# Optimization experiments

Hardware: AMD Instinct MI355X
Metric: run time of the kernel (lower is better)

Reference implementation:

```python
import jax, jax.numpy as jnp
import numpy as np

QMIN, QMAX = -128.0, 127.0

def _affine_quantize(x):
    # per-tensor asymmetric int8 activation quantization
    amin, amax = jnp.min(x), jnp.max(x)
    scale = jnp.maximum((amax - amin) / 255.0, 1e-8)
    zp = jnp.clip(jnp.round(-amin / scale) + QMIN, QMIN, QMAX)
    q = jnp.clip(jnp.round(x / scale) + zp, QMIN, QMAX)
    return q, scale, zp

def _sym_quantize(w):
    # per-tensor symmetric int8 weight quantization
    scale = jnp.maximum(jnp.max(jnp.abs(w)) / 127.0, 1e-8)
    q = jnp.clip(jnp.round(w / scale), -127.0, 127.0)
    return q, scale

def _qlinear(x, W, b):
    # quantize input -> integer GEMM (emulated in fp32) -> dequantize
    xq, sx, zx = _affine_quantize(x)
    wq, sw = _sym_quantize(W)
    acc = jnp.einsum('bsh,oh->bso', xq - zx, wq)  # int accumulate, fp32-emulated
    return acc * (sx * sw) + b


def setup_inputs() -> dict:
    key = jax.random.key(0)
    k1, k2, k3, k4, k5 = jax.random.split(key, 5)
    d, h = 1024, 4096
    x = jax.random.normal(k1, (4, 4096, d), dtype=jnp.float32)
    W1 = jax.random.normal(k2, (h, d), dtype=jnp.float32) * (1.0 / np.sqrt(d))
    b1 = jax.random.normal(k3, (h,), dtype=jnp.float32) * 0.02
    W2 = jax.random.normal(k4, (d, h), dtype=jnp.float32) * (1.0 / np.sqrt(h))
    b2 = jax.random.normal(k5, (d,), dtype=jnp.float32) * 0.02
    return {"x": x, "W1": W1, "b1": b1, "W2": W2, "b2": b2}


def reference(x, W1, b1, W2, b2):
    # 1. FP32 -> quantize -> INT8 fc1 -> dequantize -> FP32
    h = _qlinear(x, W1, b1)
    # 2. FP32 GELU (torch nn.GELU default: exact erf form); dropout p=0 is identity
    h = jax.nn.gelu(h, approximate=False)
    # 3. FP32 -> quantize -> INT8 fc2 -> dequantize -> FP32
    out = _qlinear(h, W2, b2)
    return out
```

## Files before the change

### kernel.cpp

```cpp
#include <hip/hip_runtime.h>
#include <hip/hip_bf16.h>
#include <math.h>

#define D_IN   1024
#define D_HID  4096
#define M_TOK  16384

typedef int v4i __attribute__((ext_vector_type(4)));
typedef _Float16 f16x8 __attribute__((ext_vector_type(8)));

typedef __attribute__((address_space(3))) unsigned int lds_u32;
typedef const __attribute__((address_space(1))) unsigned int glb_u32;

__device__ inline void gload_lds16(const signed char* g, signed char* l) {
    __builtin_amdgcn_global_load_lds((glb_u32*)g, (lds_u32*)l, 16, 0, 0);
}

__device__ inline float fast_erf(float x) {
    float ax = fabsf(x);
    float t = __builtin_amdgcn_rcpf(fmaf(0.3275911f, ax, 1.0f));
    float y = t * (0.254829592f +
              t * (-0.284496736f +
              t * (1.421413741f +
              t * (-1.453152027f +
              t * 1.061405429f))));
    float e = __expf(-ax * ax);
    float r = fmaf(-y, e, 1.0f);
    return copysignf(r, x);
}

#define OFF_SLOTS  ((size_t)0)
#define OFF_SCAL   ((size_t)64)
#define OFF_ISCAL  ((size_t)128)
#define OFF_XQ     ((size_t)256)
#define OFF_W1Q    (OFF_XQ  + (size_t)M_TOK * D_IN)
#define OFF_W2Q    (OFF_W1Q + (size_t)D_HID * D_IN)
#define OFF_RS1    (OFF_W2Q + (size_t)D_IN * D_HID)
#define OFF_RS2    (OFF_RS1 + (size_t)D_HID * 4)
#define OFF_H      (OFF_RS2 + (size_t)D_IN * 4 + 128)
#define OFF_HQ     (OFF_H   + (size_t)M_TOK * D_HID * 2)


__device__ inline unsigned enc_f(float f) {
    unsigned u = __float_as_uint(f);
    return (u & 0x80000000u) ? ~u : (u | 0x80000000u);
}
__device__ inline float dec_f(unsigned u) {
    return __uint_as_float((u & 0x80000000u) ? (u ^ 0x80000000u) : ~u);
}

__global__ void k_reduce_all(const float4* __restrict__ x,
                             const float4* __restrict__ w1,
                             const float4* __restrict__ w2,
                             float* __restrict__ pxmin, float* __restrict__ pxmax,
                             float* __restrict__ pw1, float* __restrict__ pw2) {
    __shared__ float red[8];
    const int b = blockIdx.x;
    const int wave = threadIdx.x >> 6, lane = threadIdx.x & 63;
    if (b < 1024) {
        float vmin = 3.4e38f, vmax = -3.4e38f;
        for (int i = b * 256 + threadIdx.x; i < M_TOK * D_IN / 4; i += 1024 * 256) {
            float4 v = x[i];
            vmin = fminf(vmin, fminf(fminf(v.x, v.y), fminf(v.z, v.w)));
            vmax = fmaxf(vmax, fmaxf(fmaxf(v.x, v.y), fmaxf(v.z, v.w)));
        }
        for (int off = 32; off > 0; off >>= 1) {
            vmin = fminf(vmin, __shfl_down(vmin, off));
            vmax = fmaxf(vmax, __shfl_down(vmax, off));
        }
        if (lane == 0) { red[wave] = vmin; red[4 + wave] = vmax; }
        __syncthreads();
        if (threadIdx.x == 0) {
            pxmin[b] = fminf(fminf(red[0], red[1]), fminf(red[2], red[3]));
            pxmax[b] = fmaxf(fmaxf(red[4], red[5]), fmaxf(red[6], red[7]));
        }
    } else {
        const float4* w = (b < 1280) ? w1 : w2;
        const int bb = (b < 1280) ? b - 1024 : b - 1280;
        float vmax = 0.0f;
        for (int i = bb * 256 + threadIdx.x; i < D_HID * D_IN / 4; i += 256 * 256) {
            float4 v = w[i];
            vmax = fmaxf(vmax, fmaxf(fmaxf(fabsf(v.x), fabsf(v.y)), fmaxf(fabsf(v.z), fabsf(v.w))));
        }
        for (int off = 32; off > 0; off >>= 1)
            vmax = fmaxf(vmax, __shfl_down(vmax, off));
        if (lane == 0) red[wave] = vmax;
        __syncthreads();
        if (threadIdx.x == 0) {
            float bm = fmaxf(fmaxf(red[0], red[1]), fmaxf(red[2], red[3]));
            if (b < 1280) pw1[bb] = bm; else pw2[bb] = bm;
        }
    }
}

__global__ void k_quant_all(const float4* __restrict__ x, int* __restrict__ xq,
                            const float* __restrict__ W1, signed char* __restrict__ w1q,
                            int* __restrict__ rs1,
                            const float* __restrict__ W2, signed char* __restrict__ w2q,
                            int* __restrict__ rs2,
                            const float* __restrict__ pxmin, const float* __restrict__ pxmax,
                            const float* __restrict__ pw1, const float* __restrict__ pw2,
                            float* __restrict__ scal, int* __restrict__ iscal,
                            unsigned* __restrict__ slots) {
    __shared__ float sred[8];
    __shared__ int red[4];
    const int b = blockIdx.x;
    const int wave = threadIdx.x >> 6, lane = threadIdx.x & 63;

    if (b < 2048) {
        float vmin = 3.4e38f, vmax = -3.4e38f;
        for (int i = threadIdx.x; i < 1024; i += 256) {
            vmin = fminf(vmin, pxmin[i]);
            vmax = fmaxf(vmax, pxmax[i]);
        }
        for (int off = 32; off > 0; off >>= 1) {
            vmin = fminf(vmin, __shfl_down(vmin, off));
            vmax = fmaxf(vmax, __shfl_down(vmax, off));
        }
        if (lane == 0) { sred[wave] = vmin; sred[4 + wave] = vmax; }
        __syncthreads();
        vmin = fminf(fminf(sred[0], sred[1]), fminf(sred[2], sred[3]));
        vmax = fmaxf(fmaxf(sred[4], sred[5]), fmaxf(sred[6], sred[7]));
        float s = fmaxf((vmax - vmin) / 255.0f, 1e-8f);
        float zp = rintf(-vmin / s) - 128.0f;
        zp = fminf(fmaxf(zp, -128.0f), 127.0f);

        if (b == 0 && threadIdx.x == 0) {
            float w1m = 0.0f, w2m = 0.0f;
            for (int i = 0; i < 256; i++) {
                w1m = fmaxf(w1m, pw1[i]);
                w2m = fmaxf(w2m, pw2[i]);
            }
            float sw1 = fmaxf(w1m / 127.0f, 1e-8f);
            float sw2 = fmaxf(w2m / 127.0f, 1e-8f);
            scal[0] = s; scal[1] = zp; scal[2] = sw1; scal[3] = sw2; scal[4] = s * sw1;
            iscal[0] = (int)zp;
            slots[4] = 0xFFFFFFFFu;
            slots[5] = 0u;
        }

        for (int i = b * 256 + threadIdx.x; i < M_TOK * D_IN / 4; i += 2048 * 256) {
            float4 v = x[i];
            int a0 = (int)fminf(fmaxf(rintf(v.x / s) + zp, -128.0f), 127.0f);
            int a1 = (int)fminf(fmaxf(rintf(v.y / s) + zp, -128.0f), 127.0f);
            int a2 = (int)fminf(fmaxf(rintf(v.z / s) + zp, -128.0f), 127.0f);
            int a3 = (int)fminf(fmaxf(rintf(v.w / s) + zp, -128.0f), 127.0f);
            xq[i] = (a0 & 255) | ((a1 & 255) << 8) | ((a2 & 255) << 16) | ((a3 & 255) << 24);
        }
        return;
    }

    const int isW1 = (b < 2048 + 4096);
    const int row = isW1 ? (b - 2048) : (b - 6144);
    const int K = isW1 ? D_IN : D_HID;
    const float* pw = isW1 ? pw1 : pw2;
    const float* W = isW1 ? W1 : W2;
    signed char* Wq = isW1 ? w1q : w2q;
    int* rsum = isW1 ? rs1 : rs2;

    float wm = pw[threadIdx.x & 255];
    for (int off = 32; off > 0; off >>= 1)
        wm = fmaxf(wm, __shfl_down(wm, off));
    if (lane == 0) sred[wave] = wm;
    __syncthreads();
    wm = fmaxf(fmaxf(sred[0], sred[1]), fmaxf(sred[2], sred[3]));
    const float s = fmaxf(wm / 127.0f, 1e-8f);

    const float4* Wr = (const float4*)(W + (size_t)row * K);
    int* out = (int*)(Wq + (size_t)row * K);
    int mysum = 0;
    for (int i = threadIdx.x; i < K / 4; i += 256) {
        float4 v = Wr[i];
        int a0 = (int)fminf(fmaxf(rintf(v.x / s), -127.0f), 127.0f);
        int a1 = (int)fminf(fmaxf(rintf(v.y / s), -127.0f), 127.0f);
        int a2 = (int)fminf(fmaxf(rintf(v.z / s), -127.0f), 127.0f);
        int a3 = (int)fminf(fmaxf(rintf(v.w / s), -127.0f), 127.0f);
        mysum += a0 + a1 + a2 + a3;
        out[i] = (a0 & 255) | ((a1 & 255) << 8) | ((a2 & 255) << 16) | ((a3 & 255) << 24);
    }
    for (int off = 32; off > 0; off >>= 1)
        mysum += __shfl_down(mysum, off);
    if (lane == 0) red[wave] = mysum;
    __syncthreads();
    if (threadIdx.x == 0) rsum[row] = red[0] + red[1] + red[2] + red[3];
}

__global__ void k_quant_h(const f16x8* __restrict__ H, int2* __restrict__ Hq, int n8,
                          const unsigned* __restrict__ slots) {
    float amin = dec_f(slots[4]), amax = dec_f(slots[5]);
    float s = fmaxf((amax - amin) / 255.0f, 1e-8f);
    float zp = rintf(-amin / s) - 128.0f;
    zp = fminf(fmaxf(zp, -128.0f), 127.0f);
    for (int i = blockIdx.x * blockDim.x + threadIdx.x; i < n8; i += gridDim.x * blockDim.x) {
        f16x8 v = H[i];
        int q[8];
#pragma unroll
        for (int j = 0; j < 8; j++)
            q[j] = ((int)fminf(fmaxf(rintf((float)v[j] / s) + zp, -128.0f), 127.0f)) & 255;
        int lo = q[0] | (q[1] << 8) | (q[2] << 16) | (q[3] << 24);
        int hi = q[4] | (q[5] << 8) | (q[6] << 16) | (q[7] << 24);
        Hq[i] = make_int2(lo, hi);
    }
}

__device__ inline void int8_mainloop256(const signed char* __restrict__ A,
                                        const signed char* __restrict__ B,
                                        int K, int m0, int n0,
                                        signed char* Ls, v4i (&acc)[8][4]) {
    const int tid = threadIdx.x;
    const int l = tid & 63, w = tid >> 6;
    const int lm = l & 15, lq = l >> 4;
    const int wmi = w >> 1, wni = w & 1;

    const int gc16 = ((l & 3) ^ ((l >> 3) & 3)) << 4;
    const int srow = (w << 4) + (l >> 2);
    const signed char* gA = A + (long)(m0 + srow) * K + gc16;
    const signed char* gB = B + (long)(n0 + srow) * K + gc16;
    const long rstep = (long)K << 6;
    signed char* lA = Ls + (w << 10) + (l << 4);
    signed char* lB = Ls + 16384 + (w << 10) + (l << 4);

    const int f16off = (lq ^ ((lm >> 1) & 3)) << 4;
    const int aoff = ((wmi << 7) + lm) * 64 + f16off;
    const int boff = 16384 + ((wni << 6) + lm) * 64 + f16off;

    const int KT = K >> 6;

    auto stage = [&](int bufoff, int kt) {
        const signed char* a = gA + ((long)kt << 6);
        const signed char* b = gB + ((long)kt << 6);
        gload_lds16(a,             lA + bufoff);
        gload_lds16(a + rstep,     lA + bufoff + 4096);
        gload_lds16(a + 2 * rstep, lA + bufoff + 8192);
        gload_lds16(a + 3 * rstep, lA + bufoff + 12288);
        gload_lds16(b,             lB + bufoff);
        gload_lds16(b + rstep,     lB + bufoff + 4096);
    };

    auto compute = [&](int bufoff) {
        v4i av[8], bv[4];
#pragma unroll
        for (int j = 0; j < 4; ++j)
            bv[j] = *(const v4i*)&Ls[bufoff + boff + j * 1024];
#pragma unroll
        for (int i = 0; i < 8; ++i)
            av[i] = *(const v4i*)&Ls[bufoff + aoff + i * 1024];
        __builtin_amdgcn_s_setprio(1);
#pragma unroll
        for (int i = 0; i < 8; ++i)
#pragma unroll
            for (int j = 0; j < 4; ++j)
                acc[i][j] = __builtin_amdgcn_mfma_i32_16x16x64_i8(av[i], bv[j], acc[i][j], 0, 0, 0);
        __builtin_amdgcn_s_setprio(0);
    };

    stage(0, 0);
    stage(24576, 1);

    int b0 = 0, b1 = 24576, b2 = 49152;
    for (int t = 0; t < KT - 2; ++t) {
        asm volatile("s_waitcnt vmcnt(6)\n\ts_barrier" ::: "memory");
        stage(b2, t + 2);
        compute(b0);
        int tmp = b0; b0 = b1; b1 = b2; b2 = tmp;
    }
    asm volatile("s_waitcnt vmcnt(6)\n\ts_barrier" ::: "memory");
    compute(b0);
    asm volatile("s_waitcnt vmcnt(0)\n\ts_barrier" ::: "memory");
    compute(b1);
}

__global__ __launch_bounds__(256, 2) void k_gemm1(const signed char* __restrict__ Aq,
                                                  const signed char* __restrict__ Bq,
                                                  _Float16* __restrict__ H,
                                                  const float* __restrict__ scal,
                                                  const int* __restrict__ iscal,
                                                  const int* __restrict__ rsum,
                                                  const float* __restrict__ bias,
                                                  unsigned* slots) {
    __shared__ __align__(16) signed char Ls[3 * 24576];
    __shared__ float red[8];
    const int nb = D_HID / 128;
    const int m0 = (blockIdx.x / nb) * 256, n0 = (blockIdx.x % nb) * 128;
    v4i acc[8][4];
    v4i zero = {0, 0, 0, 0};
#pragma unroll
    for (int i = 0; i < 8; i++)
#pragma unroll
        for (int j = 0; j < 4; j++) acc[i][j] = zero;
    int8_mainloop256(Aq, Bq, D_IN, m0, n0, Ls, acc);

    const int tid = threadIdx.x, l = tid & 63, w = tid >> 6;
    const int lm = l & 15, lq = l >> 4;
    const int wmi = w >> 1, wni = w & 1;
    float s1 = scal[4];
    int zx = iscal[0];
    float lmin = 3.4e38f, lmax = -3.4e38f;

    __syncthreads();

#pragma unroll
    for (int j = 0; j < 4; j++) {
        int n = n0 + (wni << 6) + j * 16 + lm;
        int rsn = rsum[n];
        float bn = bias[n];
        int colb = ((wni << 6) + j * 16 + lm) * 2;
#pragma unroll
        for (int i = 0; i < 8; i++) {
#pragma unroll
            for (int rg = 0; rg < 4; rg++) {
                int row = (wmi << 7) + i * 16 + lq * 4 + rg;
                int v = acc[i][j][rg] - zx * rsn;
                float fv = (float)v * s1 + bn;
                float g = fv * 0.5f * (1.0f + fast_erf(fv * 0.7071067811865476f));
                _Float16 gh = (_Float16)g;
                int off = (row * 256 + colb) ^ (((row >> 2) & 7) << 5);
                *(_Float16*)&Ls[off] = gh;
                float gf = (float)gh;
                lmin = fminf(lmin, gf);
                lmax = fmaxf(lmax, gf);
            }
        }
    }
    __syncthreads();

#pragma unroll
    for (int it = 0; it < 16; it++) {
        int row = it * 16 + (tid >> 4);
        int c = tid & 15;
        int off = (row * 256 + c * 16) ^ (((row >> 2) & 7) << 5);
        v4i d = *(const v4i*)&Ls[off];
        *(v4i*)&H[(long)(m0 + row) * D_HID + n0 + c * 8] = d;
    }

    for (int off = 32; off > 0; off >>= 1) {
        lmin = fminf(lmin, __shfl_down(lmin, off));
        lmax = fmaxf(lmax, __shfl_down(lmax, off));
    }
    if (l == 0) { red[w] = lmin; red[4 + w] = lmax; }
    __syncthreads();
    if (tid == 0) {
        atomicMin(&slots[4], enc_f(fminf(fminf(red[0], red[1]), fminf(red[2], red[3]))));
        atomicMax(&slots[5], enc_f(fmaxf(fmaxf(red[4], red[5]), fmaxf(red[6], red[7]))));
    }
}

__global__ __launch_bounds__(256, 2) void k_gemm2(const signed char* __restrict__ Aq,
                                                  const signed char* __restrict__ Bq,
                                                  float* __restrict__ Out,
                                                  const float* __restrict__ scal,
                                                  const unsigned* __restrict__ slots,
                                                  const int* __restrict__ rsum,
                                                  const float* __restrict__ bias) {
    __shared__ __align__(16) signed char Ls[3 * 24576];
    const int nb = D_IN / 128;
    const int m0 = (blockIdx.x / nb) * 256, n0 = (blockIdx.x % nb) * 128;
    v4i acc[8][4];
    v4i zero = {0, 0, 0, 0};
#pragma unroll
    for (int i = 0; i < 8; i++)
#pragma unroll
        for (int j = 0; j < 4; j++) acc[i][j] = zero;
    int8_mainloop256(Aq, Bq, D_HID, m0, n0, Ls, acc);

    const int tid = threadIdx.x, l = tid & 63, w = tid >> 6;
    const int lm = l & 15, lq = l >> 4;
    const int wmi = w >> 1, wni = w & 1;
    float amin = dec_f(slots[4]), amax = dec_f(slots[5]);
    float sh = fmaxf((amax - amin) / 255.0f, 1e-8f);
    float zpf = rintf(-amin / sh) - 128.0f;
    zpf = fminf(fmaxf(zpf, -128.0f), 127.0f);
    float s2 = sh * scal[3];
    int zx = (int)zpf;
#pragma unroll
    for (int j = 0; j < 4; j++) {
        int n = n0 + (wni << 6) + j * 16 + lm;
        int rsn = rsum[n];
        float bn = bias[n];
#pragma unroll
        for (int i = 0; i < 8; i++) {
            int mb = m0 + (wmi << 7) + i * 16 + lq * 4;
#pragma unroll
            for (int rg = 0; rg < 4; rg++) {
                int v = acc[i][j][rg] - zx * rsn;
                Out[(long)(mb + rg) * D_IN + n] = (float)v * s2 + bn;
            }
        }
    }
}

extern "C" void kernel_launch(void* const* d_in, const int* in_sizes, int n_in,
                              void* d_out, int out_size, void* d_ws, size_t ws_size,
                              hipStream_t stream) {
    const float* x  = (const float*)d_in[0];
    const float* W1 = (const float*)d_in[1];
    const float* b1 = (const float*)d_in[2];
    const float* W2 = (const float*)d_in[3];
    const float* b2 = (const float*)d_in[4];

    char* ws = (char*)d_ws;
    unsigned* slots    = (unsigned*)(ws + OFF_SLOTS);
    float* scal        = (float*)(ws + OFF_SCAL);
    int* iscal         = (int*)(ws + OFF_ISCAL);
    signed char* xq    = (signed char*)(ws + OFF_XQ);
    signed char* w1q   = (signed char*)(ws + OFF_W1Q);
    signed char* w2q   = (signed char*)(ws + OFF_W2Q);
    int* rs1           = (int*)(ws + OFF_RS1);
    int* rs2           = (int*)(ws + OFF_RS2);
    _Float16* h        = (_Float16*)(ws + OFF_H);
    signed char* hq    = (signed char*)(ws + OFF_HQ);

    float* pxmin = (float*)(ws + OFF_HQ);
    float* pxmax = pxmin + 1024;
    float* pw1   = pxmax + 1024;
    float* pw2   = pw1 + 256;

    k_reduce_all<<<1536, 256, 0, stream>>>((const float4*)x, (const float4*)W1,
                                           (const float4*)W2, pxmin, pxmax, pw1, pw2);
    k_quant_all<<<7168, 256, 0, stream>>>((const float4*)x, (int*)xq,
                                          W1, w1q, rs1, W2, w2q, rs2,
                                          pxmin, pxmax, pw1, pw2, scal, iscal, slots);
    k_gemm1<<<(M_TOK / 256) * (D_HID / 128), 256, 0, stream>>>(xq, w1q, h, scal, iscal, rs1, b1, slots);
    k_quant_h<<<4096, 256, 0, stream>>>((const f16x8*)h, (int2*)hq, M_TOK * D_HID / 8, slots);
    k_gemm2<<<(M_TOK / 256) * (D_IN / 128), 256, 0, stream>>>(hq, w2q, (float*)d_out, scal, slots, rs2, b2);
}
```

Baseline: 419.0 us.

## Fuse hidden-activation quantization into the second GEMM's A-tile loading

Removes the separate k_quant_h pass. GEMM2 now loads fp16 H tiles into registers, quantizes them to int8 and writes them to LDS, with a new double-buffered mainloop in place of the triple-buffered async global-to-LDS pipeline. This saves one full read of H plus the write and re-read of the int8 Hq buffer. In exchange, GEMM2 reads twice as many bytes for A, since each of the 8 N-blocks re-reads fp16 instead of int8. The loop also adds quantize ALU work and waits on vmcnt(0) synchronously each iteration, which lowers load/compute overlap. It also uses a reciprocal multiply in place of a division, which may differ by one ulp at rounding ties.

```diff
diff --git a/kernel.cpp b/kernel.cpp
--- a/kernel.cpp
+++ b/kernel.cpp
@@ -38,7 +38,7 @@
 #define OFF_RS1    (OFF_W2Q + (size_t)D_IN * D_HID)
 #define OFF_RS2    (OFF_RS1 + (size_t)D_HID * 4)
 #define OFF_H      (OFF_RS2 + (size_t)D_IN * 4 + 128)
-#define OFF_HQ     (OFF_H   + (size_t)M_TOK * D_HID * 2)
+#define OFF_PART   (OFF_H   + (size_t)M_TOK * D_HID * 2)
 
 
 __device__ inline unsigned enc_f(float f) {
@@ -185,24 +185,6 @@
     if (threadIdx.x == 0) rsum[row] = red[0] + red[1] + red[2] + red[3];
 }
 
-__global__ void k_quant_h(const f16x8* __restrict__ H, int2* __restrict__ Hq, int n8,
-                          const unsigned* __restrict__ slots) {
-    float amin = dec_f(slots[4]), amax = dec_f(slots[5]);
-    float s = fmaxf((amax - amin) / 255.0f, 1e-8f);
-    float zp = rintf(-amin / s) - 128.0f;
-    zp = fminf(fmaxf(zp, -128.0f), 127.0f);
-    for (int i = blockIdx.x * blockDim.x + threadIdx.x; i < n8; i += gridDim.x * blockDim.x) {
-        f16x8 v = H[i];
-        int q[8];
-#pragma unroll
-        for (int j = 0; j < 8; j++)
-            q[j] = ((int)fminf(fmaxf(rintf((float)v[j] / s) + zp, -128.0f), 127.0f)) & 255;
-        int lo = q[0] | (q[1] << 8) | (q[2] << 16) | (q[3] << 24);
-        int hi = q[4] | (q[5] << 8) | (q[6] << 16) | (q[7] << 24);
-        Hq[i] = make_int2(lo, hi);
-    }
-}
-
 __device__ inline void int8_mainloop256(const signed char* __restrict__ A,
                                         const signed char* __restrict__ B,
                                         int K, int m0, int n0,
@@ -268,6 +250,99 @@
     compute(b0);
     asm volatile("s_waitcnt vmcnt(0)\n\ts_barrier" ::: "memory");
     compute(b1);
+}
+
+__device__ inline void int8_mainloop_h(const _Float16* __restrict__ Hm,
+                                       const signed char* __restrict__ B,
+                                       int K, int m0, int n0,
+                                       float rs, float zpf,
+                                       signed char* Ls, v4i (&acc)[8][4]) {
+    const int tid = threadIdx.x;
+    const int l = tid & 63, w = tid >> 6;
+    const int lm = l & 15, lq = l >> 4;
+    const int wmi = w >> 1, wni = w & 1;
+
+    const int col0 = (l & 3) ^ ((l >> 3) & 3);
+    const int srow = (w << 4) + (l >> 2);
+    const _Float16* gA = Hm + (long)(m0 + srow) * K + col0 * 16;
+    const signed char* gB = B + (long)(n0 + srow) * K + (col0 << 4);
+    const long rstep = (long)K << 6;
+    signed char* lA = Ls + (w << 10) + (l << 4);
+    signed char* lB = Ls + 16384 + (w << 10) + (l << 4);
+
+    const int f16off = (lq ^ ((lm >> 1) & 3)) << 4;
+    const int aoff = ((wmi << 7) + lm) * 64 + f16off;
+    const int boff = 16384 + ((wni << 6) + lm) * 64 + f16off;
+    const int KT = K >> 6;
+
+    f16x8 R[4][2];
+
+    auto issue = [&](int bufoff, int kt) {
+        const _Float16* a = gA + (long)kt * 64;
+#pragma unroll
+        for (int u = 0; u < 4; ++u) {
+            R[u][0] = *(const f16x8*)(a + u * rstep);
+            R[u][1] = *(const f16x8*)(a + u * rstep + 8);
+        }
+        const signed char* b = gB + ((long)kt << 6);
+        gload_lds16(b,         lB + bufoff);
+        gload_lds16(b + rstep, lB + bufoff + 4096);
+    };
+
+    auto qwrite = [&](int bufoff) {
+#pragma unroll
+        for (int u = 0; u < 4; ++u) {
+            int qd[4];
+#pragma unroll
+            for (int d = 0; d < 4; ++d) {
+                int pk = 0;
+#pragma unroll
+                for (int e = 0; e < 4; ++e) {
+                    float h = (float)R[u][d >> 1][(d & 1) * 4 + e];
+                    float q = rintf(fmaf(h, rs, zpf));
+                    q = fminf(fmaxf(q, -128.0f), 127.0f);
+                    pk |= ((int)q & 255) << (8 * e);
+                }
+                qd[d] = pk;
+            }
+            v4i qv = { qd[0], qd[1], qd[2], qd[3] };
+            *(v4i*)(lA + bufoff + u * 4096) = qv;
+        }
+    };
+
+    auto compute = [&](int bufoff) {
+        v4i av[8], bv[4];
+#pragma unroll
+        for (int j = 0; j < 4; ++j)
+            bv[j] = *(const v4i*)&Ls[bufoff + boff + j * 1024];
+#pragma unroll
+        for (int i = 0; i < 8; ++i)
+            av[i] = *(const v4i*)&Ls[bufoff + aoff + i * 1024];
+        __builtin_amdgcn_s_setprio(1);
+#pragma unroll
+        for (int i = 0; i < 8; ++i)
+#pragma unroll
+            for (int j = 0; j < 4; ++j)
+                acc[i][j] = __builtin_amdgcn_mfma_i32_16x16x64_i8(av[i], bv[j], acc[i][j], 0, 0, 0);
+        __builtin_amdgcn_s_setprio(0);
+    };
+
+    issue(0, 0);
+    asm volatile("s_waitcnt vmcnt(0)" ::: "memory");
+    qwrite(0);
+    asm volatile("s_waitcnt lgkmcnt(0)\n\ts_barrier" ::: "memory");
+
+    for (int t = 0; t < KT; ++t) {
+        const int cur = (t & 1) * 24576;
+        const int nxt = 24576 - cur;
+        if (t + 1 < KT) issue(nxt, t + 1);
+        compute(cur);
+        if (t + 1 < KT) {
+            asm volatile("s_waitcnt vmcnt(0)" ::: "memory");
+            qwrite(nxt);
+            asm volatile("s_waitcnt lgkmcnt(0)\n\ts_barrier" ::: "memory");
+        }
+    }
 }
 
 __global__ __launch_bounds__(256, 2) void k_gemm1(const signed char* __restrict__ Aq,
@@ -345,14 +420,14 @@
     }
 }
 
-__global__ __launch_bounds__(256, 2) void k_gemm2(const signed char* __restrict__ Aq,
+__global__ __launch_bounds__(256, 2) void k_gemm2(const _Float16* __restrict__ Hm,
                                                   const signed char* __restrict__ Bq,
                                                   float* __restrict__ Out,
                                                   const float* __restrict__ scal,
                                                   const unsigned* __restrict__ slots,
                                                   const int* __restrict__ rsum,
                                                   const float* __restrict__ bias) {
-    __shared__ __align__(16) signed char Ls[3 * 24576];
+    __shared__ __align__(16) signed char Ls[2 * 24576];
     const int nb = D_IN / 128;
     const int m0 = (blockIdx.x / nb) * 256, n0 = (blockIdx.x % nb) * 128;
     v4i acc[8][4];
@@ -361,17 +436,20 @@
     for (int i = 0; i < 8; i++)
 #pragma unroll
         for (int j = 0; j < 4; j++) acc[i][j] = zero;
-    int8_mainloop256(Aq, Bq, D_HID, m0, n0, Ls, acc);
-
-    const int tid = threadIdx.x, l = tid & 63, w = tid >> 6;
-    const int lm = l & 15, lq = l >> 4;
-    const int wmi = w >> 1, wni = w & 1;
+
     float amin = dec_f(slots[4]), amax = dec_f(slots[5]);
     float sh = fmaxf((amax - amin) / 255.0f, 1e-8f);
     float zpf = rintf(-amin / sh) - 128.0f;
     zpf = fminf(fmaxf(zpf, -128.0f), 127.0f);
+    float rs = 1.0f / sh;
     float s2 = sh * scal[3];
     int zx = (int)zpf;
+
+    int8_mainloop_h(Hm, Bq, D_HID, m0, n0, rs, zpf, Ls, acc);
+
+    const int tid = threadIdx.x, l = tid & 63, w = tid >> 6;
+    const int lm = l & 15, lq = l >> 4;
+    const int wmi = w >> 1, wni = w & 1;
 #pragma unroll
     for (int j = 0; j < 4; j++) {
         int n = n0 + (wni << 6) + j * 16 + lm;
@@ -408,9 +486,8 @@
     int* rs1           = (int*)(ws + OFF_RS1);
     int* rs2           = (int*)(ws + OFF_RS2);
     _Float16* h        = (_Float16*)(ws + OFF_H);
-    signed char* hq    = (signed char*)(ws + OFF_HQ);
-
-    float* pxmin = (float*)(ws + OFF_HQ);
+
+    float* pxmin = (float*)(ws + OFF_PART);
     float* pxmax = pxmin + 1024;
     float* pw1   = pxmax + 1024;
     float* pw2   = pw1 + 256;
@@ -421,6 +498,5 @@
                                           W1, w1q, rs1, W2, w2q, rs2,
                                           pxmin, pxmax, pw1, pw2, scal, iscal, slots);
     k_gemm1<<<(M_TOK / 256) * (D_HID / 128), 256, 0, stream>>>(xq, w1q, h, scal, iscal, rs1, b1, slots);
-    k_quant_h<<<4096, 256, 0, stream>>>((const f16x8*)h, (int2*)hq, M_TOK * D_HID / 8, slots);
-    k_gemm2<<<(M_TOK / 256) * (D_IN / 128), 256, 0, stream>>>(hq, w2q, (float*)d_out, scal, slots, rs2, b2);
-}
+    k_gemm2<<<(M_TOK / 256) * (D_IN / 128), 256, 0, stream>>>(h, w2q, (float*)d_out, scal, slots, rs2, b2);
+}
```

Measured after the change: 428.3 us. +2.2%, slower.
